# Performance work log

Hardware: AMD Instinct MI355X
Metric: run time of the kernel (lower is better)

The kernel has to match this reference:

```python
import jax, jax.numpy as jnp
import numpy as np

BLOCK_SIZE = 32
NUM_PROJS = 7


def _unit_hamming(n):
    # AngularLSH._unit_hamming_distance_array (Gray-code-like permutation)
    a = np.array([0, 1], dtype=np.int32)
    for i in range(1, n):
        a = np.concatenate([a, a[::-1] + 2 ** i])
    return a


def _lsh_hash(x, proj_dir, perm, enc_vec):
    # x: [B,H,N,D], proj_dir: [1,1,D,P] -> hash ids [B,H,N]
    pd = proj_dir[0, 0]  # [D,P]
    proj = jnp.einsum('bhnd,dp->bhnp', x, pd)
    bits = (proj > 0).astype(jnp.int32)
    bin_ids = (bits * enc_vec).sum(-1)
    return perm[bin_ids]


def _causal_attn(q, k, v):
    # q,k,v: [B,N,H,D] (xformers layout), causal softmax attention
    B, N, H, D = q.shape
    s = jnp.einsum('bqhd,bkhd->bhqk', q, k) * (D ** -0.5)
    causal = jnp.tril(jnp.ones((N, N), dtype=bool))
    s = jnp.where(causal, s, jnp.finfo(s.dtype).min)
    w = jax.nn.softmax(s, axis=-1)
    return jnp.einsum('bhqk,bkhd->bqhd', w, v)


def _forward(q, k, v, proj_dir):
    B, N, H, D = q.shape
    bs = BLOCK_SIZE
    nb = N // bs
    perm = jnp.asarray(_unit_hamming(NUM_PROJS))
    enc_vec = jnp.asarray(2 ** np.arange(NUM_PROJS, dtype=np.int32))

    qt = jnp.transpose(q, (0, 2, 1, 3))  # [B,H,N,D]
    kt = jnp.transpose(k, (0, 2, 1, 3))

    q_hash = _lsh_hash(qt, proj_dir, perm, enc_vec)  # [B,H,N]
    sort_idx = jnp.argsort(q_hash, axis=2, stable=True)
    q_hash_sort = jnp.take_along_axis(q_hash, sort_idx, axis=2)
    inv_idx = jnp.argsort(sort_idx, axis=2, stable=True)
    q_sorted = jnp.take_along_axis(qt, sort_idx[..., None], axis=2)  # [B,H,N,D]

    k_hash = _lsh_hash(kt, proj_dir, perm, enc_vec)  # [B,H,N]

    # torch .view(seq_len, -1) on [B,H,N] contiguous tensors (C-order reshape)
    qh_rows = q_hash_sort.reshape(N, -1)  # [N, B*H]
    kh_rows = k_hash.reshape(N, -1)
    eq = (qh_rows == kh_rows).reshape(nb, -1)  # rows grouped by query block
    keep = (eq.sum(axis=1) > 0)  # [nb] block kept if any hash match

    # K_split_per_block = k.reshape(B, nb, -1, D) on [B,H,N,D]
    k_blocks = kt.reshape(B, nb, (H * N) // nb, D)
    k_blocks = k_blocks * keep[None, :, None, None].astype(kt.dtype)
    k_crit = k_blocks.reshape(B, H, N, D)

    # out_critical = attn(q_critical, k_critical, v_critical) then unsort
    out = _causal_attn(jnp.transpose(q_sorted, (0, 2, 1, 3)),
                       jnp.transpose(k_crit, (0, 2, 1, 3)),
                       v)  # [B,N,H,D]
    out = jnp.take_along_axis(jnp.transpose(out, (0, 2, 1, 3)), inv_idx[..., None], axis=2)
    return jnp.transpose(out, (0, 2, 1, 3))  # [B,N,H,D]


def setup_inputs() -> dict:
    key = jax.random.key(0)
    k1, k2, k3, k4 = jax.random.split(key, 4)
    B, N, H, D = 2, 2048, 16, 128
    return {
        'q': jax.random.normal(k1, (B, N, H, D), dtype=jnp.float32),
        'k': jax.random.normal(k2, (B, N, H, D), dtype=jnp.float32),
        'v': jax.random.normal(k3, (B, N, H, D), dtype=jnp.float32),
        'proj_dir': jax.random.normal(k4, (1, 1, D, NUM_PROJS), dtype=jnp.float32),
        'is_causal': 1,
        'mask': jnp.zeros((1, 1), dtype=bool),
    }


def reference(q, k, v, proj_dir, is_causal, mask):
    # is_causal is always True at every attention call site; mask is unused then.
    return _forward(q, k, v, proj_dir)
```

## Files before the change

kernel.cpp:

```cpp
#include <hip/hip_runtime.h>
#include <cstdint>

#define BB 2
#define NN 2048
#define HH 16
#define DD 128
#define BH 32
#define NPROJ 7

typedef __bf16 bf16x8 __attribute__((ext_vector_type(8)));
typedef float f32x4 __attribute__((ext_vector_type(4)));

__device__ __forceinline__ unsigned short f2bf(float f) {
  unsigned int u = __float_as_uint(f);
  u += 0x7fff + ((u >> 16) & 1);
  return (unsigned short)(u >> 16);
}

__device__ __forceinline__ bf16x8 load_q8(const float* p) {
  float4 a = *(const float4*)p;
  float4 b = *(const float4*)(p + 4);
  unsigned short r[8] = {f2bf(a.x), f2bf(a.y), f2bf(a.z), f2bf(a.w),
                         f2bf(b.x), f2bf(b.y), f2bf(b.z), f2bf(b.w)};
  return *(bf16x8*)r;
}

__global__ void prep_kernel(const float* __restrict__ q, const float* __restrict__ k,
                            const float* __restrict__ v, const float* __restrict__ pd,
                            int* __restrict__ qh, int* __restrict__ kh,
                            unsigned short* __restrict__ Vt, unsigned short* __restrict__ Kb) {
  __shared__ __align__(16) char smem[64 * 132 * 2];
  if (blockIdx.x < 4096) {
    float* spd = (float*)smem;
    for (int i = threadIdx.x; i < DD * NPROJ; i += 256) spd[i] = pd[i];
    __syncthreads();
    long long gid = (long long)blockIdx.x * 256 + threadIdx.x;
    int part = (int)(gid & 7);
    long long row = gid >> 3;
    const long long NR = (long long)BB * NN * HH;
    int isk = row >= NR;
    long long r = isk ? row - NR : row;
    const float* src = (isk ? k : q) + r * DD + part * 16;
    double acc[NPROJ];
    for (int p = 0; p < NPROJ; ++p) acc[p] = 0.0;
    __align__(16) unsigned short kb16[16];
    for (int d = 0; d < 16; d += 4) {
      float4 x = *(const float4*)(src + d);
      if (isk) {
        kb16[d + 0] = f2bf(x.x); kb16[d + 1] = f2bf(x.y);
        kb16[d + 2] = f2bf(x.z); kb16[d + 3] = f2bf(x.w);
      }
      int dbase = part * 16 + d;
      for (int p = 0; p < NPROJ; ++p) {
        acc[p] += (double)x.x * (double)spd[(dbase + 0) * NPROJ + p]
                + (double)x.y * (double)spd[(dbase + 1) * NPROJ + p]
                + (double)x.z * (double)spd[(dbase + 2) * NPROJ + p]
                + (double)x.w * (double)spd[(dbase + 3) * NPROJ + p];
      }
    }
    int b_ = (int)(r / (NN * HH));
    int rem = (int)(r % (NN * HH));
    int n_ = rem / HH, h_ = rem % HH;
    if (isk) {
      unsigned short* dst = Kb + (((long long)(b_ * HH + h_) * NN + n_) << 7) + part * 16;
      *(uint4*)dst = *(const uint4*)&kb16[0];
      *(uint4*)(dst + 8) = *(const uint4*)&kb16[8];
    }
    for (int off = 1; off < 8; off <<= 1)
      for (int p = 0; p < NPROJ; ++p) acc[p] += __shfl_xor(acc[p], off);
    if (part == 0) {
      int bin = 0;
      for (int p = 0; p < NPROJ; ++p) bin |= ((int)(acc[p] > 0.0)) << p;
      int hsh = bin ^ (bin >> 1);
      (isk ? kh : qh)[((long long)b_ * HH + h_) * NN + n_] = hsh;
    }
  } else {
    unsigned short (*tile)[132] = (unsigned short(*)[132])smem;
    int blk = blockIdx.x - 4096;
    int bh = blk >> 5;
    int n0 = (blk & 31) * 64;
    int b = bh >> 4, h = bh & 15;
    for (int it = 0; it < 8; ++it) {
      int cid = it * 256 + threadIdx.x;
      int r = cid >> 5, d4 = (cid & 31) * 4;
      float4 x = *(const float4*)(v + (((long long)(b * NN + n0 + r) * HH + h) << 7) + d4);
      *(ushort4*)&tile[r][d4] = make_ushort4(f2bf(x.x), f2bf(x.y), f2bf(x.z), f2bf(x.w));
    }
    __syncthreads();
    for (int it = 0; it < 8; ++it) {
      int cid = it * 256 + threadIdx.x;
      int d = cid >> 4, n4 = (cid & 15) * 4;
      ushort4 y = make_ushort4(tile[n4 + 0][d], tile[n4 + 1][d], tile[n4 + 2][d], tile[n4 + 3][d]);
      *(ushort4*)(Vt + ((long long)bh * DD + d) * NN + n0 + n4) = y;
    }
  }
}

__global__ void sortkeep_kernel(const int* __restrict__ qh, const int* __restrict__ kh,
                                int* __restrict__ sidx, int* __restrict__ keep) {
  __shared__ int sh[NN];
  __shared__ int cnt[4][128];
  __shared__ int cum[128];
  __shared__ int kflag[2];
  int bh = blockIdx.x;
  const int* src = qh + (long long)bh * NN;
  for (int i = threadIdx.x; i < NN; i += 512) sh[i] = src[i];
  if (threadIdx.x < 2) kflag[threadIdx.x] = 0;
  __syncthreads();
  int bin = threadIdx.x & 127, seg = threadIdx.x >> 7;
  int n0 = seg * (NN / 4);
  int c = 0;
  for (int n = n0; n < n0 + NN / 4; ++n) c += (sh[n] == bin);
  cnt[seg][bin] = c;
  __syncthreads();
  if (threadIdx.x == 0) {
    int run = 0;
    for (int t = 0; t < 128; ++t) {
      cum[t] = run;
      run += cnt[0][t] + cnt[1][t] + cnt[2][t] + cnt[3][t];
    }
  }
  __syncthreads();
  int pos = cum[bin];
  for (int s = 0; s < seg; ++s) pos += cnt[s][bin];
  int f0 = 0, f1 = 0;
  for (int n = n0; n < n0 + NN / 4; ++n)
    if (sh[n] == bin) {
      sidx[(long long)bh * NN + pos] = n;
      int match = (bin == kh[(long long)bh * NN + pos]);
      if (pos < 1024) f0 |= match; else f1 |= match;
      ++pos;
    }
  if (f0) atomicOr(&kflag[0], 1);
  if (f1) atomicOr(&kflag[1], 1);
  __syncthreads();
  if (threadIdx.x < 2) keep[bh * 2 + threadIdx.x] = kflag[threadIdx.x];
}

__global__ __launch_bounds__(256, 3)
void flash_kernel(const float* __restrict__ q, const unsigned short* __restrict__ Kb,
                  const unsigned short* __restrict__ Vt, const int* __restrict__ sidx,
                  const int* __restrict__ keep, float* __restrict__ out) {
  __shared__ __align__(16) unsigned short Kt[64 * 136];
  __shared__ __align__(16) unsigned short Vs[128 * 72];
  __shared__ __align__(16) unsigned short Pb[4][16 * 72];

  int bh = blockIdx.x;
  int qt = 31 - (int)blockIdx.y;
  int b = bh >> 4, h = bh & 15;
  int tid = threadIdx.x;
  int w = tid >> 6, lane = tid & 63;
  int l16 = lane & 15, qd = lane >> 4;

  const unsigned short* Kh = Kb + (long long)bh * NN * DD;
  const unsigned short* Vb = Vt + (long long)bh * DD * NN;
  const float scale = 0.088388347648318447f;

  const int ksr = tid >> 4;
  const int ksc = (tid & 15) * 8;
  const int vsr = tid >> 3;
  const int vsc = (tid & 7) * 8;

  uint4 kreg[4], vreg[4];

#define STAGE_LOAD(K0, KP)                                                            \
  {                                                                                   \
    if (KP) {                                                                         \
      _Pragma("unroll")                                                               \
      for (int it = 0; it < 4; ++it)                                                  \
        kreg[it] = *(const uint4*)(Kh + (long long)((K0) + it * 16 + ksr) * DD + ksc);\
    } else {                                                                          \
      _Pragma("unroll")                                                               \
      for (int it = 0; it < 4; ++it) kreg[it] = make_uint4(0, 0, 0, 0);               \
    }                                                                                 \
    _Pragma("unroll")                                                                 \
    for (int it = 0; it < 4; ++it)                                                    \
      vreg[it] = *(const uint4*)(Vb + (long long)(it * 32 + vsr) * NN + (K0) + vsc);  \
  }

#define STAGE_WRITE()                                                                 \
  {                                                                                   \
    _Pragma("unroll")                                                                 \
    for (int it = 0; it < 4; ++it)                                                    \
      *(uint4*)&Kt[(it * 16 + ksr) * 136 + ksc] = kreg[it];                           \
    _Pragma("unroll")                                                                 \
    for (int it = 0; it < 4; ++it)                                                    \
      *(uint4*)&Vs[(it * 32 + vsr) * 72 + vsc] = vreg[it];                            \
  }

  int qrow = qt * 64 + w * 16 + l16;

  bf16x8 qf[4];
  {
    int nq = sidx[bh * NN + qrow];
    const float* p0 = q + (((long long)(b * NN + nq) * HH + h) << 7) + qd * 8;
#pragma unroll
    for (int c = 0; c < 4; ++c) qf[c] = load_q8(p0 + c * 32);
  }
  f32x4 o[8];
#pragma unroll
  for (int i = 0; i < 8; ++i) o[i] = (f32x4){0.f, 0.f, 0.f, 0.f};
  float m = -__builtin_inff(), l = 0.f;

  STAGE_LOAD(0, keep[h * 4]);
  STAGE_WRITE();
  __syncthreads();

  for (int kb = 0; kb <= qt; ++kb) {
    if (kb < qt) STAGE_LOAD((kb + 1) * 64, keep[h * 4 + ((kb + 1) >> 3)]);

    int k0 = kb * 64;

    float s[16];
    __builtin_amdgcn_s_setprio(1);
#pragma unroll
    for (int t = 0; t < 4; ++t) {
      f32x4 a1 = (f32x4){0.f, 0.f, 0.f, 0.f};
#pragma unroll
      for (int c = 0; c < 4; ++c) {
        bf16x8 kf = *(const bf16x8*)&Kt[(t * 16 + l16) * 136 + c * 32 + qd * 8];
        a1 = __builtin_amdgcn_mfma_f32_16x16x32_bf16(kf, qf[c], a1, 0, 0, 0);
      }
      if (kb == qt) {
#pragma unroll
        for (int r = 0; r < 4; ++r) {
          int keyg = k0 + t * 16 + qd * 4 + r;
          s[t * 4 + r] = (keyg > qrow) ? -__builtin_inff() : a1[r] * scale;
        }
      } else {
#pragma unroll
        for (int r = 0; r < 4; ++r) s[t * 4 + r] = a1[r] * scale;
      }
    }
    __builtin_amdgcn_s_setprio(0);

    {
      float x0 = fmaxf(fmaxf(s[0], s[1]), fmaxf(s[2], s[3]));
      float x1 = fmaxf(fmaxf(s[4], s[5]), fmaxf(s[6], s[7]));
      float x2 = fmaxf(fmaxf(s[8], s[9]), fmaxf(s[10], s[11]));
      float x3 = fmaxf(fmaxf(s[12], s[13]), fmaxf(s[14], s[15]));
      float mloc = fmaxf(fmaxf(x0, x1), fmaxf(x2, x3));
      mloc = fmaxf(mloc, __shfl_xor(mloc, 16));
      mloc = fmaxf(mloc, __shfl_xor(mloc, 32));
      if (__any(mloc > m)) {
        float mnew = fmaxf(m, mloc);
        float alpha = __expf(m - mnew);
        float aO[4];
#pragma unroll
        for (int r = 0; r < 4; ++r) aO[r] = __shfl(alpha, qd * 4 + r);
#pragma unroll
        for (int c8 = 0; c8 < 8; ++c8)
#pragma unroll
          for (int r = 0; r < 4; ++r) o[c8][r] *= aO[r];
        l *= alpha;
        m = mnew;
      }
      float psum = 0.f;
#pragma unroll
      for (int t = 0; t < 4; ++t) {
        float p0 = __expf(s[t * 4 + 0] - m);
        float p1 = __expf(s[t * 4 + 1] - m);
        float p2 = __expf(s[t * 4 + 2] - m);
        float p3 = __expf(s[t * 4 + 3] - m);
        psum += (p0 + p1) + (p2 + p3);
        *(ushort4*)&Pb[w][l16 * 72 + t * 16 + qd * 4] =
            make_ushort4(f2bf(p0), f2bf(p1), f2bf(p2), f2bf(p3));
      }
      psum += __shfl_xor(psum, 16);
      psum += __shfl_xor(psum, 32);
      l += psum;
    }

    __builtin_amdgcn_s_setprio(1);
#pragma unroll
    for (int g = 0; g < 2; ++g) {
      bf16x8 pf = *(const bf16x8*)&Pb[w][l16 * 72 + g * 32 + qd * 8];
#pragma unroll
      for (int c8 = 0; c8 < 8; ++c8) {
        bf16x8 vf = *(const bf16x8*)&Vs[(c8 * 16 + l16) * 72 + g * 32 + qd * 8];
        o[c8] = __builtin_amdgcn_mfma_f32_16x16x32_bf16(pf, vf, o[c8], 0, 0, 0);
      }
    }
    __builtin_amdgcn_s_setprio(0);

    if (kb < qt) {
      __syncthreads();
      STAGE_WRITE();
      __syncthreads();
    }
  }

  float lO[4];
  int nO[4];
#pragma unroll
  for (int r = 0; r < 4; ++r) {
    lO[r] = __shfl(l, qd * 4 + r);
    nO[r] = sidx[(long long)bh * NN + qt * 64 + w * 16 + qd * 4 + r];
  }
#pragma unroll
  for (int r = 0; r < 4; ++r) {
    float inv = 1.f / lO[r];
    float* ob = out + (((long long)(b * NN + nO[r]) * HH + h) << 7) + l16;
#pragma unroll
    for (int c8 = 0; c8 < 8; ++c8)
      ob[c8 * 16] = o[c8][r] * inv;
  }
#undef STAGE_LOAD
#undef STAGE_WRITE
}

extern "C" void kernel_launch(void* const* d_in, const int* in_sizes, int n_in,
                              void* d_out, int out_size, void* d_ws, size_t ws_size,
                              hipStream_t stream) {
  const float* q = (const float*)d_in[0];
  const float* k = (const float*)d_in[1];
  const float* v = (const float*)d_in[2];
  const float* pd = (const float*)d_in[3];
  float* out = (float*)d_out;
  char* ws = (char*)d_ws;
  int* qh   = (int*)(ws + 0);
  int* kh   = (int*)(ws + (1u << 18));
  int* sidx = (int*)(ws + (2u << 18));
  int* keep = (int*)(ws + 3u * (1u << 18));
  unsigned short* Vt = (unsigned short*)(ws + (2u << 20));
  unsigned short* Kb = (unsigned short*)(ws + (18u << 20));

  prep_kernel<<<5120, 256, 0, stream>>>(q, k, v, pd, qh, kh, Vt, Kb);
  sortkeep_kernel<<<32, 512, 0, stream>>>(qh, kh, sidx, keep);
  flash_kernel<<<dim3(32, 32), 256, 0, stream>>>(q, Kb, Vt, sidx, keep, out);
}
```

Measured before the change: 344.1 us.

## Split long causal query tiles across key halves with a combine pass, use exp2

Query tiles in the upper half of the causal triangle now have their key range split into two blocks. Each block writes unnormalized partial O, m and l to workspace, and a new combine kernel merges the two halves. The goal is to balance the triangular workload and shorten the tail set by the longest tiles. The softmax scale is folded into an exp2 argument via fma. The sort kernel also doubles to 1024 threads with 8 segments. In exchange there is an extra kernel launch and partial-result traffic through global memory, and the split depends on workspace size.

Measured after the change: 348.1 us. About the same (+1.2%).

```diff
diff --git a/kernel.cpp b/kernel.cpp
--- a/kernel.cpp
+++ b/kernel.cpp
@@ -24,6 +24,15 @@
                          f2bf(b.x), f2bf(b.y), f2bf(b.z), f2bf(b.w)};
   return *(bf16x8*)r;
 }
+
+#if __has_builtin(__builtin_amdgcn_exp2f)
+#define EXP2(x) __builtin_amdgcn_exp2f(x)
+#else
+#define EXP2(x) exp2f(x)
+#endif
+
+#define CEXPC 0.1275174316582815f
+#define PSLOT 8320
 
 __global__ void prep_kernel(const float* __restrict__ q, const float* __restrict__ k,
                             const float* __restrict__ v, const float* __restrict__ pd,
@@ -99,32 +108,33 @@
 __global__ void sortkeep_kernel(const int* __restrict__ qh, const int* __restrict__ kh,
                                 int* __restrict__ sidx, int* __restrict__ keep) {
   __shared__ int sh[NN];
-  __shared__ int cnt[4][128];
+  __shared__ int cnt[8][128];
   __shared__ int cum[128];
   __shared__ int kflag[2];
   int bh = blockIdx.x;
   const int* src = qh + (long long)bh * NN;
-  for (int i = threadIdx.x; i < NN; i += 512) sh[i] = src[i];
+  for (int i = threadIdx.x; i < NN; i += 1024) sh[i] = src[i];
   if (threadIdx.x < 2) kflag[threadIdx.x] = 0;
   __syncthreads();
   int bin = threadIdx.x & 127, seg = threadIdx.x >> 7;
-  int n0 = seg * (NN / 4);
+  int n0 = seg * (NN / 8);
   int c = 0;
-  for (int n = n0; n < n0 + NN / 4; ++n) c += (sh[n] == bin);
+  for (int n = n0; n < n0 + NN / 8; ++n) c += (sh[n] == bin);
   cnt[seg][bin] = c;
   __syncthreads();
   if (threadIdx.x == 0) {
     int run = 0;
     for (int t = 0; t < 128; ++t) {
       cum[t] = run;
-      run += cnt[0][t] + cnt[1][t] + cnt[2][t] + cnt[3][t];
+      run += cnt[0][t] + cnt[1][t] + cnt[2][t] + cnt[3][t]
+           + cnt[4][t] + cnt[5][t] + cnt[6][t] + cnt[7][t];
     }
   }
   __syncthreads();
   int pos = cum[bin];
   for (int s = 0; s < seg; ++s) pos += cnt[s][bin];
   int f0 = 0, f1 = 0;
-  for (int n = n0; n < n0 + NN / 4; ++n)
+  for (int n = n0; n < n0 + NN / 8; ++n)
     if (sh[n] == bin) {
       sidx[(long long)bh * NN + pos] = n;
       int match = (bin == kh[(long long)bh * NN + pos]);
@@ -140,13 +150,28 @@
 __global__ __launch_bounds__(256, 3)
 void flash_kernel(const float* __restrict__ q, const unsigned short* __restrict__ Kb,
                   const unsigned short* __restrict__ Vt, const int* __restrict__ sidx,
-                  const int* __restrict__ keep, float* __restrict__ out) {
+                  const int* __restrict__ keep, float* __restrict__ out,
+                  float* __restrict__ part, int split_qt) {
   __shared__ __align__(16) unsigned short Kt[64 * 136];
   __shared__ __align__(16) unsigned short Vs[128 * 72];
   __shared__ __align__(16) unsigned short Pb[4][16 * 72];
 
   int bh = blockIdx.x;
-  int qt = 31 - (int)blockIdx.y;
+  int nsp = 32 - split_qt;
+  int y = blockIdx.y;
+  int qt, kb0, kb1, half;
+  if (y < 2 * nsp) {
+    half = y & 1;
+    qt = 31 - (y >> 1);
+    int nk = qt + 1, mid = nk >> 1;
+    kb0 = half ? mid : 0;
+    kb1 = half ? nk : mid;
+  } else {
+    half = -1;
+    qt = split_qt - 1 - (y - 2 * nsp);
+    kb0 = 0;
+    kb1 = qt + 1;
+  }
   int b = bh >> 4, h = bh & 15;
   int tid = threadIdx.x;
   int w = tid >> 6, lane = tid & 63;
@@ -154,7 +179,6 @@
 
   const unsigned short* Kh = Kb + (long long)bh * NN * DD;
   const unsigned short* Vb = Vt + (long long)bh * DD * NN;
-  const float scale = 0.088388347648318447f;
 
   const int ksr = tid >> 4;
   const int ksc = (tid & 15) * 8;
@@ -202,12 +226,12 @@
   for (int i = 0; i < 8; ++i) o[i] = (f32x4){0.f, 0.f, 0.f, 0.f};
   float m = -__builtin_inff(), l = 0.f;
 
-  STAGE_LOAD(0, keep[h * 4]);
+  STAGE_LOAD(kb0 * 64, keep[h * 4 + (kb0 >> 3)]);
   STAGE_WRITE();
   __syncthreads();
 
-  for (int kb = 0; kb <= qt; ++kb) {
-    if (kb < qt) STAGE_LOAD((kb + 1) * 64, keep[h * 4 + ((kb + 1) >> 3)]);
+  for (int kb = kb0; kb < kb1; ++kb) {
+    if (kb + 1 < kb1) STAGE_LOAD((kb + 1) * 64, keep[h * 4 + ((kb + 1) >> 3)]);
 
     int k0 = kb * 64;
 
@@ -225,11 +249,11 @@
 #pragma unroll
         for (int r = 0; r < 4; ++r) {
           int keyg = k0 + t * 16 + qd * 4 + r;
-          s[t * 4 + r] = (keyg > qrow) ? -__builtin_inff() : a1[r] * scale;
+          s[t * 4 + r] = (keyg > qrow) ? -__builtin_inff() : a1[r];
         }
       } else {
 #pragma unroll
-        for (int r = 0; r < 4; ++r) s[t * 4 + r] = a1[r] * scale;
+        for (int r = 0; r < 4; ++r) s[t * 4 + r] = a1[r];
       }
     }
     __builtin_amdgcn_s_setprio(0);
@@ -244,7 +268,7 @@
       mloc = fmaxf(mloc, __shfl_xor(mloc, 32));
       if (__any(mloc > m)) {
         float mnew = fmaxf(m, mloc);
-        float alpha = __expf(m - mnew);
+        float alpha = EXP2((m - mnew) * CEXPC);
         float aO[4];
 #pragma unroll
         for (int r = 0; r < 4; ++r) aO[r] = __shfl(alpha, qd * 4 + r);
@@ -255,13 +279,14 @@
         l *= alpha;
         m = mnew;
       }
+      float mc = m * CEXPC;
       float psum = 0.f;
 #pragma unroll
       for (int t = 0; t < 4; ++t) {
-        float p0 = __expf(s[t * 4 + 0] - m);
-        float p1 = __expf(s[t * 4 + 1] - m);
-        float p2 = __expf(s[t * 4 + 2] - m);
-        float p3 = __expf(s[t * 4 + 3] - m);
+        float p0 = EXP2(__builtin_fmaf(s[t * 4 + 0], CEXPC, -mc));
+        float p1 = EXP2(__builtin_fmaf(s[t * 4 + 1], CEXPC, -mc));
+        float p2 = EXP2(__builtin_fmaf(s[t * 4 + 2], CEXPC, -mc));
+        float p3 = EXP2(__builtin_fmaf(s[t * 4 + 3], CEXPC, -mc));
         psum += (p0 + p1) + (p2 + p3);
         *(ushort4*)&Pb[w][l16 * 72 + t * 16 + qd * 4] =
             make_ushort4(f2bf(p0), f2bf(p1), f2bf(p2), f2bf(p3));
@@ -283,30 +308,81 @@
     }
     __builtin_amdgcn_s_setprio(0);
 
-    if (kb < qt) {
+    if (kb + 1 < kb1) {
       __syncthreads();
       STAGE_WRITE();
       __syncthreads();
     }
   }
 
-  float lO[4];
-  int nO[4];
-#pragma unroll
-  for (int r = 0; r < 4; ++r) {
-    lO[r] = __shfl(l, qd * 4 + r);
-    nO[r] = sidx[(long long)bh * NN + qt * 64 + w * 16 + qd * 4 + r];
-  }
-#pragma unroll
-  for (int r = 0; r < 4; ++r) {
-    float inv = 1.f / lO[r];
-    float* ob = out + (((long long)(b * NN + nO[r]) * HH + h) << 7) + l16;
-#pragma unroll
-    for (int c8 = 0; c8 < 8; ++c8)
-      ob[c8 * 16] = o[c8][r] * inv;
+  if (half >= 0) {
+    float* ps = part + (long long)((bh * nsp + (qt - split_qt)) * 2 + half) * PSLOT;
+#pragma unroll
+    for (int r = 0; r < 4; ++r) {
+      int row = w * 16 + qd * 4 + r;
+      float* pr = ps + row * 128 + l16;
+#pragma unroll
+      for (int c8 = 0; c8 < 8; ++c8) pr[c8 * 16] = o[c8][r];
+    }
+    if (qd == 0) {
+      int row = w * 16 + l16;
+      ps[8192 + row] = m;
+      ps[8256 + row] = l;
+    }
+  } else {
+    float lO[4];
+    int nO[4];
+#pragma unroll
+    for (int r = 0; r < 4; ++r) {
+      lO[r] = __shfl(l, qd * 4 + r);
+      nO[r] = sidx[(long long)bh * NN + qt * 64 + w * 16 + qd * 4 + r];
+    }
+#pragma unroll
+    for (int r = 0; r < 4; ++r) {
+      float inv = 1.f / lO[r];
+      float* ob = out + (((long long)(b * NN + nO[r]) * HH + h) << 7) + l16;
+#pragma unroll
+      for (int c8 = 0; c8 < 8; ++c8)
+        ob[c8 * 16] = o[c8][r] * inv;
+    }
   }
 #undef STAGE_LOAD
 #undef STAGE_WRITE
+}
+
+__global__ __launch_bounds__(256)
+void combine_kernel(const float* __restrict__ part, const int* __restrict__ sidx,
+                    float* __restrict__ out, int split_qt) {
+  int nsp = 32 - split_qt;
+  int bh = blockIdx.x & 31, qi = blockIdx.x >> 5;
+  int qt = split_qt + qi;
+  int b = bh >> 4, h = bh & 15;
+  const float* p0 = part + (long long)((bh * nsp + qi) * 2 + 0) * PSLOT;
+  const float* p1 = p0 + PSLOT;
+  int row = threadIdx.x >> 2;
+  int colg = (threadIdx.x & 3) * 32;
+  float m0 = p0[8192 + row], l0 = p0[8256 + row];
+  float m1 = p1[8192 + row], l1 = p1[8256 + row];
+  float M = fmaxf(m0, m1);
+  float a0 = EXP2((m0 - M) * CEXPC);
+  float a1 = EXP2((m1 - M) * CEXPC);
+  float inv = 1.f / (a0 * l0 + a1 * l1);
+  float s0 = a0 * inv, s1 = a1 * inv;
+  int nO = sidx[(long long)bh * NN + qt * 64 + row];
+  float* ob = out + (((long long)(b * NN + nO) * HH + h) << 7) + colg;
+  const float* r0 = p0 + row * 128 + colg;
+  const float* r1 = p1 + row * 128 + colg;
+#pragma unroll
+  for (int c = 0; c < 32; c += 4) {
+    float4 x0 = *(const float4*)(r0 + c);
+    float4 x1 = *(const float4*)(r1 + c);
+    float4 yv;
+    yv.x = s0 * x0.x + s1 * x1.x;
+    yv.y = s0 * x0.y + s1 * x1.y;
+    yv.z = s0 * x0.z + s1 * x1.z;
+    yv.w = s0 * x0.w + s1 * x1.w;
+    *(float4*)(ob + c) = yv;
+  }
 }
 
 extern "C" void kernel_launch(void* const* d_in, const int* in_sizes, int n_in,
@@ -324,8 +400,19 @@
   int* keep = (int*)(ws + 3u * (1u << 18));
   unsigned short* Vt = (unsigned short*)(ws + (2u << 20));
   unsigned short* Kb = (unsigned short*)(ws + (18u << 20));
+  size_t pbase = 34ull << 20;
+  float* part = (float*)(ws + pbase);
+
+  int split_qt;
+  if (ws_size >= pbase + 32ull * 16 * 2 * (PSLOT * 4)) split_qt = 16;
+  else if (ws_size >= pbase + 32ull * 8 * 2 * (PSLOT * 4)) split_qt = 24;
+  else split_qt = 32;
+  int nsp = 32 - split_qt;
 
   prep_kernel<<<5120, 256, 0, stream>>>(q, k, v, pd, qh, kh, Vt, Kb);
-  sortkeep_kernel<<<32, 512, 0, stream>>>(qh, kh, sidx, keep);
-  flash_kernel<<<dim3(32, 32), 256, 0, stream>>>(q, Kb, Vt, sidx, keep, out);
-}
+  sortkeep_kernel<<<32, 1024, 0, stream>>>(qh, kh, sidx, keep);
+  flash_kernel<<<dim3(32, 2 * nsp + split_qt), 256, 0, stream>>>(
+      q, Kb, Vt, sidx, keep, out, part, split_qt);
+  if (nsp > 0)
+    combine_kernel<<<32 * nsp, 256, 0, stream>>>(part, sidx, out, split_qt);
+}
```
